# Kernel tuning notes

Measured on AMD Instinct MI355X. Metric: run time of the kernel, lower is better.

The kernel has to match this reference:

```python
import jax, jax.numpy as jnp
import numpy as np

H = 64
IN = 4
B = 256
T = 2048

def _uniform(key, shape, k):
    return jax.random.uniform(key, shape, jnp.float32, -k, k)

def setup_inputs() -> dict:
    key = jax.random.key(0)
    ks = jax.random.split(key, 12)
    k = 1.0 / np.sqrt(H)
    x = jax.random.normal(ks[0], (B, T, IN), jnp.float32)
    # bidirectional layer 1 (forward + backward directions); biases fused (b_ih + b_hh)
    Wih_f = _uniform(ks[1], (4 * H, IN), k); Whh_f = _uniform(ks[2], (4 * H, H), k); b_f = _uniform(ks[3], (4 * H,), k)
    Wih_b = _uniform(ks[4], (4 * H, IN), k); Whh_b = _uniform(ks[5], (4 * H, H), k); b_b = _uniform(ks[6], (4 * H,), k)
    # unidirectional layer 2, input 2H
    Wih2 = _uniform(ks[7], (4 * H, 2 * H), k); Whh2 = _uniform(ks[8], (4 * H, H), k); b2 = _uniform(ks[9], (4 * H,), k)
    Wfc = _uniform(ks[10], (1, H), k); bfc = _uniform(ks[11], (1,), k)
    return {"x": x, "Wih_f": Wih_f, "Whh_f": Whh_f, "b_f": b_f,
            "Wih_b": Wih_b, "Whh_b": Whh_b, "b_b": b_b,
            "Wih2": Wih2, "Whh2": Whh2, "b2": b2, "Wfc": Wfc, "bfc": bfc}

def _run_lstm(x, Wih, Whh, b, reverse=False):
    # x: [B, T, D] -> outputs [B, T, H], final h [B, H]
    bsz = x.shape[0]
    hdim = Whh.shape[1]
    pre = jnp.einsum('btd,gd->btg', x, Wih) + b  # [B, T, 4H], input contribution precomputed
    pre = jnp.swapaxes(pre, 0, 1)                # [T, B, 4H]
    h0 = jnp.zeros((bsz, hdim), x.dtype)
    c0 = jnp.zeros((bsz, hdim), x.dtype)
    def step(carry, p):
        h, c = carry
        g = p + h @ Whh.T
        i, f, gg, o = jnp.split(g, 4, axis=-1)  # torch gate order: i, f, g, o
        i = jax.nn.sigmoid(i); f = jax.nn.sigmoid(f)
        gg = jnp.tanh(gg); o = jax.nn.sigmoid(o)
        c = f * c + i * gg
        h = o * jnp.tanh(c)
        return (h, c), h
    (hn, _), hs = jax.lax.scan(step, (h0, c0), pre, reverse=reverse)
    return jnp.swapaxes(hs, 0, 1), hn  # [B, T, H], [B, H]

def reference(x, Wih_f, Whh_f, b_f, Wih_b, Whh_b, b_b, Wih2, Whh2, b2, Wfc, bfc):
    out_f, _ = _run_lstm(x, Wih_f, Whh_f, b_f, reverse=False)
    out_b, _ = _run_lstm(x, Wih_b, Whh_b, b_b, reverse=True)
    out1 = jnp.concatenate([out_f, out_b], axis=-1)  # [B, T, 2H]
    _, hn2 = _run_lstm(out1, Wih2, Whh2, b2, reverse=False)  # final hidden [B, H]
    logits = hn2 @ Wfc.T + bfc  # [B, 1]
    return logits
```

## Files before the change

kernel.cpp:

```cpp
#include <hip/hip_runtime.h>

#define HDIM 64
#define BATCH 256
#define TLEN 2048
#define CH 16

__device__ __forceinline__ float rcp_fast(float x) { return __builtin_amdgcn_rcpf(x); }
__device__ __forceinline__ float sigmoid_fast(float x) { return rcp_fast(1.0f + __expf(-x)); }
__device__ __forceinline__ float tanh_fast(float x)    { return 1.0f - 2.0f * rcp_fast(1.0f + __expf(2.0f * x)); }

__device__ __forceinline__ float dpp_xor1_add(float x) {
    int v = __builtin_amdgcn_update_dpp(0, __float_as_int(x), 0xB1, 0xF, 0xF, true);
    return x + __int_as_float(v);
}
__device__ __forceinline__ float dpp_xor2_add(float x) {
    int v = __builtin_amdgcn_update_dpp(0, __float_as_int(x), 0x4E, 0xF, 0xF, true);
    return x + __int_as_float(v);
}
__device__ __forceinline__ float swz_xor4_add(float x) {
    int v = __builtin_amdgcn_ds_swizzle(__float_as_int(x), 0x101F);
    return x + __int_as_float(v);
}
__device__ __forceinline__ float dot4(float4 a, float4 b, float acc) {
    acc = fmaf(a.x, b.x, acc); acc = fmaf(a.y, b.y, acc);
    acc = fmaf(a.z, b.z, acc); acc = fmaf(a.w, b.w, acc);
    return acc;
}

__global__ __launch_bounds__(256, 2)
void lstm_layer1(const float* __restrict__ x,
                 const float* __restrict__ Wih_f, const float* __restrict__ Whh_f, const float* __restrict__ b_f,
                 const float* __restrict__ Wih_b, const float* __restrict__ Whh_b, const float* __restrict__ b_b,
                 float* __restrict__ out1)
{
    const int bidx = blockIdx.x >> 1;
    const int dir  = blockIdx.x & 1;
    const float* __restrict__ Wih = dir ? Wih_b : Wih_f;
    const float* __restrict__ Whh = dir ? Whh_b : Whh_f;
    const float* __restrict__ bb  = dir ? b_b   : b_f;

    const int tid = threadIdx.x;
    const int u   = tid >> 2;
    const int p   = tid & 3;

    __shared__ float xlds[TLEN * 4];
    __shared__ float hbuf[2][HDIM];

    {
        const float4* src = (const float4*)(x + (size_t)bidx * TLEN * 4);
        float4* dst = (float4*)xlds;
        #pragma unroll
        for (int i = 0; i < 8; ++i) dst[tid + 256 * i] = src[tid + 256 * i];
    }
    if (tid < 2 * HDIM) ((float*)hbuf)[tid] = 0.f;

    const float* wbase = Whh + (size_t)u * HDIM + 16 * p;
    const float4 W00 = *(const float4*)(wbase + 0*4096 +  0), W01 = *(const float4*)(wbase + 0*4096 +  4),
                 W02 = *(const float4*)(wbase + 0*4096 +  8), W03 = *(const float4*)(wbase + 0*4096 + 12);
    const float4 W10 = *(const float4*)(wbase + 1*4096 +  0), W11 = *(const float4*)(wbase + 1*4096 +  4),
                 W12 = *(const float4*)(wbase + 1*4096 +  8), W13 = *(const float4*)(wbase + 1*4096 + 12);
    const float4 W20 = *(const float4*)(wbase + 2*4096 +  0), W21 = *(const float4*)(wbase + 2*4096 +  4),
                 W22 = *(const float4*)(wbase + 2*4096 +  8), W23 = *(const float4*)(wbase + 2*4096 + 12);
    const float4 W30 = *(const float4*)(wbase + 3*4096 +  0), W31 = *(const float4*)(wbase + 3*4096 +  4),
                 W32 = *(const float4*)(wbase + 3*4096 +  8), W33 = *(const float4*)(wbase + 3*4096 + 12);
    const float4 I0 = *(const float4*)(Wih + (0*64 + u) * 4);
    const float4 I1 = *(const float4*)(Wih + (1*64 + u) * 4);
    const float4 I2 = *(const float4*)(Wih + (2*64 + u) * 4);
    const float4 I3 = *(const float4*)(Wih + (3*64 + u) * 4);
    const float b0 = bb[u], b1 = bb[64 + u], b2g = bb[128 + u], b3 = bb[192 + u];
    __syncthreads();

    float c = 0.f;
    const float* xp = xlds + (dir ? (TLEN - 1) * 4 : 0);
    const int xstep = dir ? -4 : 4;
    float* outp = out1 + (size_t)bidx * TLEN * (2 * HDIM)
                + (size_t)(dir ? (TLEN - 1) : 0) * (2 * HDIM) + dir * HDIM + u;
    const ptrdiff_t ostep = dir ? -(2 * HDIM) : (2 * HDIM);

    #pragma unroll 2
    for (int s = 0; s < TLEN; ++s) {
        const float* hb = hbuf[s & 1];
        const float4 h0 = *(const float4*)(hb + 16 * p + 0);
        const float4 h1 = *(const float4*)(hb + 16 * p + 4);
        const float4 h2 = *(const float4*)(hb + 16 * p + 8);
        const float4 h3 = *(const float4*)(hb + 16 * p + 12);

        float g0 = dot4(W03, h3, dot4(W02, h2, dot4(W01, h1, dot4(W00, h0, 0.f))));
        float g1 = dot4(W13, h3, dot4(W12, h2, dot4(W11, h1, dot4(W10, h0, 0.f))));
        float g2 = dot4(W23, h3, dot4(W22, h2, dot4(W21, h1, dot4(W20, h0, 0.f))));
        float g3 = dot4(W33, h3, dot4(W32, h2, dot4(W31, h1, dot4(W30, h0, 0.f))));

        g0 = dpp_xor2_add(dpp_xor1_add(g0));
        g1 = dpp_xor2_add(dpp_xor1_add(g1));
        g2 = dpp_xor2_add(dpp_xor1_add(g2));
        g3 = dpp_xor2_add(dpp_xor1_add(g3));

        const float4 xv = *(const float4*)xp;
        g0 += dot4(I0, xv, b0);
        g1 += dot4(I1, xv, b1);
        g2 += dot4(I2, xv, b2g);
        g3 += dot4(I3, xv, b3);

        const float ig = sigmoid_fast(g0);
        const float fg = sigmoid_fast(g1);
        const float gg = tanh_fast(g2);
        const float og = sigmoid_fast(g3);
        c = fmaf(fg, c, ig * gg);
        const float h = og * tanh_fast(c);

        if (p == 0) {
            hbuf[(s & 1) ^ 1][u] = h;
            *outp = h;
        }
        outp += ostep;
        xp   += xstep;
        __syncthreads();
    }
}

__global__ __launch_bounds__(512, 2)
void lstm_layer2(const float* __restrict__ out1,
                 const float* __restrict__ Wih2, const float* __restrict__ Whh2, const float* __restrict__ bias2,
                 const float* __restrict__ Wfc, const float* __restrict__ bfc,
                 float* __restrict__ out)
{
    const int bidx = blockIdx.x;
    const int tid  = threadIdx.x;
    const int w    = tid >> 6;
    const int lane = tid & 63;
    const int ul   = lane >> 3;
    const int p8   = lane & 7;
    const int u    = w * 8 + ul;
    const int rot  = p8 >> 1;

    __shared__ float inbuf[2][CH][2 * HDIM];
    __shared__ float hbuf[2][HDIM];

    const float* whbase = Whh2 + (size_t)u * HDIM + 8 * p8;
    const float4 H00 = *(const float4*)(whbase + 0*4096 + 0), H01 = *(const float4*)(whbase + 0*4096 + 4);
    const float4 H10 = *(const float4*)(whbase + 1*4096 + 0), H11 = *(const float4*)(whbase + 1*4096 + 4);
    const float4 H20 = *(const float4*)(whbase + 2*4096 + 0), H21 = *(const float4*)(whbase + 2*4096 + 4);
    const float4 H30 = *(const float4*)(whbase + 3*4096 + 0), H31 = *(const float4*)(whbase + 3*4096 + 4);
    const float* wibase = Wih2 + (size_t)u * 128 + 16 * p8;
    #define LWI(g, j) *(const float4*)(wibase + (g)*8192 + ((((j) + rot) & 3) << 2))
    const float4 X00 = LWI(0,0), X01 = LWI(0,1), X02 = LWI(0,2), X03 = LWI(0,3);
    const float4 X10 = LWI(1,0), X11 = LWI(1,1), X12 = LWI(1,2), X13 = LWI(1,3);
    const float4 X20 = LWI(2,0), X21 = LWI(2,1), X22 = LWI(2,2), X23 = LWI(2,3);
    const float4 X30 = LWI(3,0), X31 = LWI(3,1), X32 = LWI(3,2), X33 = LWI(3,3);
    #undef LWI
    const float b0 = bias2[u], b1 = bias2[64 + u], b2g = bias2[128 + u], b3 = bias2[192 + u];

    if (tid < 2 * HDIM) ((float*)hbuf)[tid] = 0.f;

    const float4* src = (const float4*)(out1 + (size_t)bidx * TLEN * (2 * HDIM));
    ((float4*)&inbuf[0][0][0])[tid] = src[tid];
    __syncthreads();

    float c = 0.f;

    for (int chunk = 0; chunk < TLEN / CH; ++chunk) {
        const int cb = chunk & 1;
        const bool havenext = (chunk + 1 < TLEN / CH);
        float4 pf;
        if (havenext) pf = src[(size_t)(chunk + 1) * 512 + tid];

        #pragma unroll 2
        for (int ts = 0; ts < CH; ++ts) {
            const int s = chunk * CH + ts;
            const float* hb = hbuf[s & 1];
            const float* xr = &inbuf[cb][ts][16 * p8];

            const float4 x0 = *(const float4*)(xr + (((0 + rot) & 3) << 2));
            const float4 x1 = *(const float4*)(xr + (((1 + rot) & 3) << 2));
            const float4 x2 = *(const float4*)(xr + (((2 + rot) & 3) << 2));
            const float4 x3 = *(const float4*)(xr + (((3 + rot) & 3) << 2));
            const float4 h0 = *(const float4*)(hb + 8 * p8 + 0);
            const float4 h1 = *(const float4*)(hb + 8 * p8 + 4);

            float g0 = dot4(H01, h1, dot4(H00, h0, dot4(X03, x3, dot4(X02, x2, dot4(X01, x1, dot4(X00, x0, 0.f))))));
            float g1 = dot4(H11, h1, dot4(H10, h0, dot4(X13, x3, dot4(X12, x2, dot4(X11, x1, dot4(X10, x0, 0.f))))));
            float g2 = dot4(H21, h1, dot4(H20, h0, dot4(X23, x3, dot4(X22, x2, dot4(X21, x1, dot4(X20, x0, 0.f))))));
            float g3 = dot4(H31, h1, dot4(H30, h0, dot4(X33, x3, dot4(X32, x2, dot4(X31, x1, dot4(X30, x0, 0.f))))));

            g0 = swz_xor4_add(dpp_xor2_add(dpp_xor1_add(g0))) + b0;
            g1 = swz_xor4_add(dpp_xor2_add(dpp_xor1_add(g1))) + b1;
            g2 = swz_xor4_add(dpp_xor2_add(dpp_xor1_add(g2))) + b2g;
            g3 = swz_xor4_add(dpp_xor2_add(dpp_xor1_add(g3))) + b3;

            const float ig = sigmoid_fast(g0);
            const float fg = sigmoid_fast(g1);
            const float gg = tanh_fast(g2);
            const float og = sigmoid_fast(g3);
            c = fmaf(fg, c, ig * gg);
            const float h = og * tanh_fast(c);

            if (p8 == 0) hbuf[(s & 1) ^ 1][u] = h;
            __syncthreads();
        }
        if (havenext) {
            ((float4*)&inbuf[cb ^ 1][0][0])[tid] = pf;
            __syncthreads();
        }
    }

    if (w == 0) {
        float part = hbuf[0][lane] * Wfc[lane];
        #pragma unroll
        for (int m = 1; m < 64; m <<= 1) part += __shfl_xor(part, m, 64);
        if (lane == 0) out[bidx] = part + bfc[0];
    }
}

extern "C" void kernel_launch(void* const* d_in, const int* in_sizes, int n_in,
                              void* d_out, int out_size, void* d_ws, size_t ws_size,
                              hipStream_t stream) {
    const float* x     = (const float*)d_in[0];
    const float* Wih_f = (const float*)d_in[1];
    const float* Whh_f = (const float*)d_in[2];
    const float* b_f   = (const float*)d_in[3];
    const float* Wih_b = (const float*)d_in[4];
    const float* Whh_b = (const float*)d_in[5];
    const float* b_b   = (const float*)d_in[6];
    const float* Wih2  = (const float*)d_in[7];
    const float* Whh2  = (const float*)d_in[8];
    const float* b2    = (const float*)d_in[9];
    const float* Wfc   = (const float*)d_in[10];
    const float* bfc   = (const float*)d_in[11];

    float* out1 = (float*)d_ws;

    lstm_layer1<<<dim3(2 * BATCH), dim3(256), 0, stream>>>(
        x, Wih_f, Whh_f, b_f, Wih_b, Whh_b, b_b, out1);
    lstm_layer2<<<dim3(BATCH), dim3(512), 0, stream>>>(
        out1, Wih2, Whh2, b2, Wfc, bfc, (float*)d_out);
}
```

Baseline: 2.215 ms.

## Double threads per hidden unit and split gate activations across lanes

Both LSTM kernels now use twice as many threads per hidden unit: 8 lanes in layer 1 and 16 in layer 2. Each lane does a shorter dot product and computes the activation for only one gate, with the four gate values exchanged by cross-lane shuffles in a shared epilogue. The goal is a shorter serial per-timestep critical path (fewer FMAs and one transcendental per lane instead of four). The cost is larger blocks, extra shuffle and reduction steps, and more threads taking part in each per-step __syncthreads. The layer-2 input chunk grows to 32 timesteps to match the 1024-thread block.

```diff
diff --git a/kernel.cpp b/kernel.cpp
--- a/kernel.cpp
+++ b/kernel.cpp
@@ -3,7 +3,7 @@
 #define HDIM 64
 #define BATCH 256
 #define TLEN 2048
-#define CH 16
+#define CH 32
 
 __device__ __forceinline__ float rcp_fast(float x) { return __builtin_amdgcn_rcpf(x); }
 __device__ __forceinline__ float sigmoid_fast(float x) { return rcp_fast(1.0f + __expf(-x)); }
@@ -27,7 +27,22 @@
     return acc;
 }
 
-__global__ __launch_bounds__(256, 2)
+__device__ __forceinline__ float cell_epilogue(float G, float c, int q, float* hout) {
+    const float act = (q == 2) ? tanh_fast(G) : sigmoid_fast(G);
+    const float a1 = __shfl_xor(act, 1, 64);
+    const float a2 = __shfl_xor(act, 2, 64);
+    const float a3 = __shfl_xor(act, 3, 64);
+    const bool qb0 = (q & 1), qb1 = (q & 2);
+    const float pe = qb0 ? a1 : act, po = qb0 ? act : a1;
+    const float oe = qb0 ? a3 : a2,  oo = qb0 ? a2 : a3;
+    const float gi = qb1 ? oe : pe,  gf = qb1 ? oo : po;
+    const float gg = qb1 ? pe : oe,  go = qb1 ? po : oo;
+    const float cn = fmaf(gf, c, gi * gg);
+    *hout = go * tanh_fast(cn);
+    return cn;
+}
+
+__global__ __launch_bounds__(512, 4)
 void lstm_layer1(const float* __restrict__ x,
                  const float* __restrict__ Wih_f, const float* __restrict__ Whh_f, const float* __restrict__ b_f,
                  const float* __restrict__ Wih_b, const float* __restrict__ Whh_b, const float* __restrict__ b_b,
@@ -40,8 +55,9 @@
     const float* __restrict__ bb  = dir ? b_b   : b_f;
 
     const int tid = threadIdx.x;
-    const int u   = tid >> 2;
-    const int p   = tid & 3;
+    const int u   = tid >> 3;
+    const int L   = tid & 7;
+    const int q   = L & 3;
 
     __shared__ float xlds[TLEN * 4];
     __shared__ float hbuf[2][HDIM];
@@ -50,24 +66,17 @@
         const float4* src = (const float4*)(x + (size_t)bidx * TLEN * 4);
         float4* dst = (float4*)xlds;
         #pragma unroll
-        for (int i = 0; i < 8; ++i) dst[tid + 256 * i] = src[tid + 256 * i];
+        for (int i = 0; i < 4; ++i) dst[tid + 512 * i] = src[tid + 512 * i];
     }
     if (tid < 2 * HDIM) ((float*)hbuf)[tid] = 0.f;
 
-    const float* wbase = Whh + (size_t)u * HDIM + 16 * p;
-    const float4 W00 = *(const float4*)(wbase + 0*4096 +  0), W01 = *(const float4*)(wbase + 0*4096 +  4),
-                 W02 = *(const float4*)(wbase + 0*4096 +  8), W03 = *(const float4*)(wbase + 0*4096 + 12);
-    const float4 W10 = *(const float4*)(wbase + 1*4096 +  0), W11 = *(const float4*)(wbase + 1*4096 +  4),
-                 W12 = *(const float4*)(wbase + 1*4096 +  8), W13 = *(const float4*)(wbase + 1*4096 + 12);
-    const float4 W20 = *(const float4*)(wbase + 2*4096 +  0), W21 = *(const float4*)(wbase + 2*4096 +  4),
-                 W22 = *(const float4*)(wbase + 2*4096 +  8), W23 = *(const float4*)(wbase + 2*4096 + 12);
-    const float4 W30 = *(const float4*)(wbase + 3*4096 +  0), W31 = *(const float4*)(wbase + 3*4096 +  4),
-                 W32 = *(const float4*)(wbase + 3*4096 +  8), W33 = *(const float4*)(wbase + 3*4096 + 12);
-    const float4 I0 = *(const float4*)(Wih + (0*64 + u) * 4);
-    const float4 I1 = *(const float4*)(Wih + (1*64 + u) * 4);
-    const float4 I2 = *(const float4*)(Wih + (2*64 + u) * 4);
-    const float4 I3 = *(const float4*)(Wih + (3*64 + u) * 4);
-    const float b0 = bb[u], b1 = bb[64 + u], b2g = bb[128 + u], b3 = bb[192 + u];
+    const float* wbase = Whh + (size_t)u * HDIM + 8 * L;
+    const float4 W0a = *(const float4*)(wbase + 0*4096 + 0), W0b = *(const float4*)(wbase + 0*4096 + 4);
+    const float4 W1a = *(const float4*)(wbase + 1*4096 + 0), W1b = *(const float4*)(wbase + 1*4096 + 4);
+    const float4 W2a = *(const float4*)(wbase + 2*4096 + 0), W2b = *(const float4*)(wbase + 2*4096 + 4);
+    const float4 W3a = *(const float4*)(wbase + 3*4096 + 0), W3b = *(const float4*)(wbase + 3*4096 + 4);
+    const float4 Iq = *(const float4*)(Wih + (size_t)(q * 64 + u) * 4);
+    const float  bq = bb[q * 64 + u];
     __syncthreads();
 
     float c = 0.f;
@@ -80,35 +89,28 @@
     #pragma unroll 2
     for (int s = 0; s < TLEN; ++s) {
         const float* hb = hbuf[s & 1];
-        const float4 h0 = *(const float4*)(hb + 16 * p + 0);
-        const float4 h1 = *(const float4*)(hb + 16 * p + 4);
-        const float4 h2 = *(const float4*)(hb + 16 * p + 8);
-        const float4 h3 = *(const float4*)(hb + 16 * p + 12);
-
-        float g0 = dot4(W03, h3, dot4(W02, h2, dot4(W01, h1, dot4(W00, h0, 0.f))));
-        float g1 = dot4(W13, h3, dot4(W12, h2, dot4(W11, h1, dot4(W10, h0, 0.f))));
-        float g2 = dot4(W23, h3, dot4(W22, h2, dot4(W21, h1, dot4(W20, h0, 0.f))));
-        float g3 = dot4(W33, h3, dot4(W32, h2, dot4(W31, h1, dot4(W30, h0, 0.f))));
-
-        g0 = dpp_xor2_add(dpp_xor1_add(g0));
-        g1 = dpp_xor2_add(dpp_xor1_add(g1));
-        g2 = dpp_xor2_add(dpp_xor1_add(g2));
-        g3 = dpp_xor2_add(dpp_xor1_add(g3));
+        const float4 h0 = *(const float4*)(hb + 8 * L + 0);
+        const float4 h1 = *(const float4*)(hb + 8 * L + 4);
+
+        float p0 = dot4(W0b, h1, dot4(W0a, h0, 0.f));
+        float p1 = dot4(W1b, h1, dot4(W1a, h0, 0.f));
+        float p2 = dot4(W2b, h1, dot4(W2a, h0, 0.f));
+        float p3 = dot4(W3b, h1, dot4(W3a, h0, 0.f));
+
+        p0 = dpp_xor2_add(dpp_xor1_add(p0));
+        p1 = dpp_xor2_add(dpp_xor1_add(p1));
+        p2 = dpp_xor2_add(dpp_xor1_add(p2));
+        p3 = dpp_xor2_add(dpp_xor1_add(p3));
+        float G = (q == 0) ? p0 : (q == 1) ? p1 : (q == 2) ? p2 : p3;
+        G = swz_xor4_add(G);
 
         const float4 xv = *(const float4*)xp;
-        g0 += dot4(I0, xv, b0);
-        g1 += dot4(I1, xv, b1);
-        g2 += dot4(I2, xv, b2g);
-        g3 += dot4(I3, xv, b3);
-
-        const float ig = sigmoid_fast(g0);
-        const float fg = sigmoid_fast(g1);
-        const float gg = tanh_fast(g2);
-        const float og = sigmoid_fast(g3);
-        c = fmaf(fg, c, ig * gg);
-        const float h = og * tanh_fast(c);
-
-        if (p == 0) {
+        G = dot4(Iq, xv, G + bq);
+
+        float h;
+        c = cell_epilogue(G, c, q, &h);
+
+        if (L == 3) {
             hbuf[(s & 1) ^ 1][u] = h;
             *outp = h;
         }
@@ -118,7 +120,7 @@
     }
 }
 
-__global__ __launch_bounds__(512, 2)
+__global__ __launch_bounds__(1024, 4)
 void lstm_layer2(const float* __restrict__ out1,
                  const float* __restrict__ Wih2, const float* __restrict__ Whh2, const float* __restrict__ bias2,
                  const float* __restrict__ Wfc, const float* __restrict__ bfc,
@@ -126,34 +128,29 @@
 {
     const int bidx = blockIdx.x;
     const int tid  = threadIdx.x;
-    const int w    = tid >> 6;
-    const int lane = tid & 63;
-    const int ul   = lane >> 3;
-    const int p8   = lane & 7;
-    const int u    = w * 8 + ul;
-    const int rot  = p8 >> 1;
-
-    __shared__ float inbuf[2][CH][2 * HDIM];
+    const int u    = tid >> 4;
+    const int L    = tid & 15;
+    const int q    = L & 3;
+
+    __shared__ float xbuf[2][CH][2 * HDIM];
     __shared__ float hbuf[2][HDIM];
 
-    const float* whbase = Whh2 + (size_t)u * HDIM + 8 * p8;
-    const float4 H00 = *(const float4*)(whbase + 0*4096 + 0), H01 = *(const float4*)(whbase + 0*4096 + 4);
-    const float4 H10 = *(const float4*)(whbase + 1*4096 + 0), H11 = *(const float4*)(whbase + 1*4096 + 4);
-    const float4 H20 = *(const float4*)(whbase + 2*4096 + 0), H21 = *(const float4*)(whbase + 2*4096 + 4);
-    const float4 H30 = *(const float4*)(whbase + 3*4096 + 0), H31 = *(const float4*)(whbase + 3*4096 + 4);
-    const float* wibase = Wih2 + (size_t)u * 128 + 16 * p8;
-    #define LWI(g, j) *(const float4*)(wibase + (g)*8192 + ((((j) + rot) & 3) << 2))
-    const float4 X00 = LWI(0,0), X01 = LWI(0,1), X02 = LWI(0,2), X03 = LWI(0,3);
-    const float4 X10 = LWI(1,0), X11 = LWI(1,1), X12 = LWI(1,2), X13 = LWI(1,3);
-    const float4 X20 = LWI(2,0), X21 = LWI(2,1), X22 = LWI(2,2), X23 = LWI(2,3);
-    const float4 X30 = LWI(3,0), X31 = LWI(3,1), X32 = LWI(3,2), X33 = LWI(3,3);
-    #undef LWI
-    const float b0 = bias2[u], b1 = bias2[64 + u], b2g = bias2[128 + u], b3 = bias2[192 + u];
+    const float* whbase = Whh2 + (size_t)u * HDIM + 4 * L;
+    const float4 H0 = *(const float4*)(whbase + 0*4096);
+    const float4 H1 = *(const float4*)(whbase + 1*4096);
+    const float4 H2 = *(const float4*)(whbase + 2*4096);
+    const float4 H3 = *(const float4*)(whbase + 3*4096);
+    const float* wibase = Wih2 + (size_t)u * 128 + 8 * L;
+    const float4 X0a = *(const float4*)(wibase + 0*8192 + 0), X0b = *(const float4*)(wibase + 0*8192 + 4);
+    const float4 X1a = *(const float4*)(wibase + 1*8192 + 0), X1b = *(const float4*)(wibase + 1*8192 + 4);
+    const float4 X2a = *(const float4*)(wibase + 2*8192 + 0), X2b = *(const float4*)(wibase + 2*8192 + 4);
+    const float4 X3a = *(const float4*)(wibase + 3*8192 + 0), X3b = *(const float4*)(wibase + 3*8192 + 4);
+    const float bq = bias2[q * 64 + u];
 
     if (tid < 2 * HDIM) ((float*)hbuf)[tid] = 0.f;
 
     const float4* src = (const float4*)(out1 + (size_t)bidx * TLEN * (2 * HDIM));
-    ((float4*)&inbuf[0][0][0])[tid] = src[tid];
+    ((float4*)&xbuf[0][0][0])[tid] = src[tid];
     __syncthreads();
 
     float c = 0.f;
@@ -162,52 +159,49 @@
         const int cb = chunk & 1;
         const bool havenext = (chunk + 1 < TLEN / CH);
         float4 pf;
-        if (havenext) pf = src[(size_t)(chunk + 1) * 512 + tid];
+        if (havenext) pf = src[(size_t)(chunk + 1) * 1024 + tid];
 
         #pragma unroll 2
         for (int ts = 0; ts < CH; ++ts) {
             const int s = chunk * CH + ts;
             const float* hb = hbuf[s & 1];
-            const float* xr = &inbuf[cb][ts][16 * p8];
-
-            const float4 x0 = *(const float4*)(xr + (((0 + rot) & 3) << 2));
-            const float4 x1 = *(const float4*)(xr + (((1 + rot) & 3) << 2));
-            const float4 x2 = *(const float4*)(xr + (((2 + rot) & 3) << 2));
-            const float4 x3 = *(const float4*)(xr + (((3 + rot) & 3) << 2));
-            const float4 h0 = *(const float4*)(hb + 8 * p8 + 0);
-            const float4 h1 = *(const float4*)(hb + 8 * p8 + 4);
-
-            float g0 = dot4(H01, h1, dot4(H00, h0, dot4(X03, x3, dot4(X02, x2, dot4(X01, x1, dot4(X00, x0, 0.f))))));
-            float g1 = dot4(H11, h1, dot4(H10, h0, dot4(X13, x3, dot4(X12, x2, dot4(X11, x1, dot4(X10, x0, 0.f))))));
-            float g2 = dot4(H21, h1, dot4(H20, h0, dot4(X23, x3, dot4(X22, x2, dot4(X21, x1, dot4(X20, x0, 0.f))))));
-            float g3 = dot4(H31, h1, dot4(H30, h0, dot4(X33, x3, dot4(X32, x2, dot4(X31, x1, dot4(X30, x0, 0.f))))));
-
-            g0 = swz_xor4_add(dpp_xor2_add(dpp_xor1_add(g0))) + b0;
-            g1 = swz_xor4_add(dpp_xor2_add(dpp_xor1_add(g1))) + b1;
-            g2 = swz_xor4_add(dpp_xor2_add(dpp_xor1_add(g2))) + b2g;
-            g3 = swz_xor4_add(dpp_xor2_add(dpp_xor1_add(g3))) + b3;
-
-            const float ig = sigmoid_fast(g0);
-            const float fg = sigmoid_fast(g1);
-            const float gg = tanh_fast(g2);
-            const float og = sigmoid_fast(g3);
-            c = fmaf(fg, c, ig * gg);
-            const float h = og * tanh_fast(c);
-
-            if (p8 == 0) hbuf[(s & 1) ^ 1][u] = h;
+            const float* xr = &xbuf[cb][ts][8 * L];
+
+            const float4 x0 = *(const float4*)(xr + 0);
+            const float4 x1 = *(const float4*)(xr + 4);
+            const float4 hv = *(const float4*)(hb + 4 * L);
+
+            float p0 = dot4(H0, hv, dot4(X0b, x1, dot4(X0a, x0, 0.f)));
+            float p1 = dot4(H1, hv, dot4(X1b, x1, dot4(X1a, x0, 0.f)));
+            float p2 = dot4(H2, hv, dot4(X2b, x1, dot4(X2a, x0, 0.f)));
+            float p3 = dot4(H3, hv, dot4(X3b, x1, dot4(X3a, x0, 0.f)));
+
+            p0 = dpp_xor2_add(dpp_xor1_add(p0));
+            p1 = dpp_xor2_add(dpp_xor1_add(p1));
+            p2 = dpp_xor2_add(dpp_xor1_add(p2));
+            p3 = dpp_xor2_add(dpp_xor1_add(p3));
+            float G = (q == 0) ? p0 : (q == 1) ? p1 : (q == 2) ? p2 : p3;
+            G = swz_xor4_add(G);
+            G += __shfl_xor(G, 8, 64);
+            G += bq;
+
+            float h;
+            c = cell_epilogue(G, c, q, &h);
+
+            if (L == 3) hbuf[(s & 1) ^ 1][u] = h;
             __syncthreads();
         }
         if (havenext) {
-            ((float4*)&inbuf[cb ^ 1][0][0])[tid] = pf;
+            ((float4*)&xbuf[cb ^ 1][0][0])[tid] = pf;
             __syncthreads();
         }
     }
 
-    if (w == 0) {
-        float part = hbuf[0][lane] * Wfc[lane];
+    if (tid < 64) {
+        float part = hbuf[0][tid] * Wfc[tid];
         #pragma unroll
         for (int m = 1; m < 64; m <<= 1) part += __shfl_xor(part, m, 64);
-        if (lane == 0) out[bidx] = part + bfc[0];
+        if (tid == 0) out[bidx] = part + bfc[0];
     }
 }
 
@@ -229,8 +223,8 @@
 
     float* out1 = (float*)d_ws;
 
-    lstm_layer1<<<dim3(2 * BATCH), dim3(256), 0, stream>>>(
+    lstm_layer1<<<dim3(2 * BATCH), dim3(512), 0, stream>>>(
         x, Wih_f, Whh_f, b_f, Wih_b, Whh_b, b_b, out1);
-    lstm_layer2<<<dim3(BATCH), dim3(512), 0, stream>>>(
+    lstm_layer2<<<dim3(BATCH), dim3(1024), 0, stream>>>(
         out1, Wih2, Whh2, b2, Wfc, bfc, (float*)d_out);
 }
```

New measurement: 2.675 ms. 1.21x slower.
